# Performance work log

Hardware: AMD Instinct MI355X
Metric: run time of the kernel (lower is better)

## Reference

```python
import jax, jax.numpy as jnp
import numpy as np

B, N, D, H = 4, 1024, 512, 8
DH = D // H  # per-head dim for V and for each of the two Q/K halves
LAM = 0.5


def setup_inputs() -> dict:
    key = jax.random.key(0)
    ks = jax.random.split(key, 7)
    s = 0.02
    return {
        "x": jax.random.normal(ks[0], (B, N, D), dtype=jnp.float32),
        "Wq": jax.random.normal(ks[1], (D, 2 * D), dtype=jnp.float32) * s,
        "bq": jax.random.normal(ks[2], (2 * D,), dtype=jnp.float32) * s,
        "Wk": jax.random.normal(ks[3], (D, 2 * D), dtype=jnp.float32) * s,
        "bk": jax.random.normal(ks[4], (2 * D,), dtype=jnp.float32) * s,
        "Wv": jax.random.normal(ks[5], (D, D), dtype=jnp.float32) * s,
        "bv": jax.random.normal(ks[6], (D,), dtype=jnp.float32) * s,
    }


def reference(x, Wq, bq, Wk, bk, Wv, bv):
    b, n, d = x.shape
    q = (x @ Wq + bq).reshape(b, n, H, 2 * DH).transpose(0, 2, 1, 3)  # [B,H,N,2*DH]
    k = (x @ Wk + bk).reshape(b, n, H, 2 * DH).transpose(0, 2, 1, 3)
    v = (x @ Wv + bv).reshape(b, n, H, DH).transpose(0, 2, 1, 3)      # [B,H,N,DH]
    q1, q2 = q[..., :DH], q[..., DH:]
    k1, k2 = k[..., :DH], k[..., DH:]
    scale = 1.0 / jnp.sqrt(jnp.float32(DH))
    a1 = jax.nn.softmax(jnp.einsum("bhqd,bhkd->bhqk", q1, k1) * scale, axis=-1)
    a2 = jax.nn.softmax(jnp.einsum("bhqd,bhkd->bhqk", q2, k2) * scale, axis=-1)
    attn = a1 - LAM * a2                                              # [B,H,N,N]
    out = jnp.einsum("bhqk,bhkd->bhqd", attn, v)                      # [B,H,N,DH]
    return out.transpose(0, 2, 1, 3).reshape(b, n, d)
```

## Files before the change

kernel.cpp:

```cpp
#include <hip/hip_runtime.h>
#include <hip/hip_bf16.h>

typedef unsigned short u16;
typedef short s16x8 __attribute__((ext_vector_type(8)));
typedef float f32x4 __attribute__((ext_vector_type(4)));

__device__ inline u16 f2bf(float f) {
  union { float f; unsigned int u; } v; v.f = f;
  unsigned int r = v.u + 0x7fffu + ((v.u >> 16) & 1u);
  return (u16)(r >> 16);
}

__device__ __forceinline__ void g2lds16(const u16* g, u16* l) {
  __builtin_amdgcn_global_load_lds((const __attribute__((address_space(1))) void*)g,
                                   (__attribute__((address_space(3))) void*)l, 16, 0, 0);
}

__global__ __launch_bounds__(256) void cast_x_kernel(const float* __restrict__ x,
                                                     u16* __restrict__ xb) {
  int i = (blockIdx.x * 256 + threadIdx.x) * 8;
  float4 a = *(const float4*)(x + i);
  float4 b = *(const float4*)(x + i + 4);
  s16x8 o;
  o[0] = (short)f2bf(a.x); o[1] = (short)f2bf(a.y);
  o[2] = (short)f2bf(a.z); o[3] = (short)f2bf(a.w);
  o[4] = (short)f2bf(b.x); o[5] = (short)f2bf(b.y);
  o[6] = (short)f2bf(b.z); o[7] = (short)f2bf(b.w);
  *(s16x8*)(xb + i) = o;
}

__global__ __launch_bounds__(256) void transpose_cast_w(const float* __restrict__ src, int C,
                                                        int rowoff, u16* __restrict__ wt) {
  __shared__ float tile[64][65];
  int j0 = blockIdx.x * 64, k0 = blockIdx.y * 64;
  int tx = threadIdx.x % 64, ty4 = threadIdx.x / 64;
#pragma unroll
  for (int p = 0; p < 16; ++p) {
    int r = p * 4 + ty4;
    tile[r][tx] = src[(size_t)(k0 + r) * C + j0 + tx];
  }
  __syncthreads();
#pragma unroll
  for (int p = 0; p < 16; ++p) {
    int r = p * 4 + ty4;
    wt[(size_t)(rowoff + j0 + r) * 512 + k0 + tx] = f2bf(tile[tx][r]);
  }
}

__global__ __launch_bounds__(256, 2) void gemm_qkv(const u16* __restrict__ xb, const u16* __restrict__ wt,
                                                   const float* __restrict__ bq, const float* __restrict__ bk,
                                                   const float* __restrict__ bv,
                                                   u16* __restrict__ qa, u16* __restrict__ ka,
                                                   u16* __restrict__ va) {
  __shared__ __align__(16) u16 As[128 * 64];
  __shared__ __align__(16) u16 Bs[128 * 64];
  int m0 = blockIdx.x * 128, j0 = blockIdx.y * 128;
  int tid = threadIdx.x;
  int w = tid >> 6, lane = tid & 63, quad = lane >> 4, l16 = lane & 15;
  int wr = (w >> 1) * 64, wc = (w & 1) * 64;

  int srow[4], scol[4], sbase[4];
#pragma unroll
  for (int it = 0; it < 4; ++it) {
    int s = it * 256 + tid;
    srow[it] = s >> 3;
    scol[it] = (s & 7) ^ ((s >> 3) & 7);
    sbase[it] = (s & ~63) * 8;
  }

  f32x4 acc[4][4];
#pragma unroll
  for (int i = 0; i < 4; ++i)
#pragma unroll
    for (int j = 0; j < 4; ++j)
#pragma unroll
      for (int r = 0; r < 4; ++r) acc[i][j][r] = 0.f;

  for (int kk = 0; kk < 8; ++kk) {
    int k0 = kk * 64;
    __syncthreads();
#pragma unroll
    for (int it = 0; it < 4; ++it) {
      g2lds16(xb + (size_t)(m0 + srow[it]) * 512 + k0 + scol[it] * 8, &As[sbase[it]]);
      g2lds16(wt + (size_t)(j0 + srow[it]) * 512 + k0 + scol[it] * 8, &Bs[sbase[it]]);
    }
    __syncthreads();
#pragma unroll
    for (int kb = 0; kb < 2; ++kb) {
      s16x8 af[4], bfr[4];
#pragma unroll
      for (int rb = 0; rb < 4; ++rb) {
        int row = wr + rb * 16 + l16;
        af[rb] = *(const s16x8*)(&As[row * 64 + (((kb * 4 + quad) ^ (row & 7)) * 8)]);
      }
#pragma unroll
      for (int cb = 0; cb < 4; ++cb) {
        int row = wc + cb * 16 + l16;
        bfr[cb] = *(const s16x8*)(&Bs[row * 64 + (((kb * 4 + quad) ^ (row & 7)) * 8)]);
      }
#pragma unroll
      for (int rb = 0; rb < 4; ++rb)
#pragma unroll
        for (int cb = 0; cb < 4; ++cb)
          acc[rb][cb] = __builtin_amdgcn_mfma_f32_16x16x32_bf16(af[rb], bfr[cb], acc[rb][cb], 0, 0, 0);
    }
  }

#pragma unroll
  for (int cb = 0; cb < 4; ++cb) {
    int j = j0 + wc + cb * 16 + l16;
    float bias = (j < 1024) ? bq[j] : (j < 2048) ? bk[j - 1024] : bv[j - 2048];
#pragma unroll
    for (int rb = 0; rb < 4; ++rb) {
#pragma unroll
      for (int r = 0; r < 4; ++r) {
        int m = m0 + wr + rb * 16 + quad * 4 + r;
        int bidx = m >> 10, n = m & 1023;
        u16 o = f2bf(acc[rb][cb][r] + bias);
        if (j < 1024) {
          int h = j >> 7, r2 = j & 127;
          qa[((size_t)((bidx * 8 + h) * 1024 + n)) * 128 + r2] = o;
        } else if (j < 2048) {
          int jj = j - 1024, h = jj >> 7, r2 = jj & 127;
          ka[((size_t)((bidx * 8 + h) * 1024 + n)) * 128 + r2] = o;
        } else {
          int jj = j - 2048, h = jj >> 6, d = jj & 63;
          va[((size_t)((bidx * 8 + h) * 64 + d)) * 1024 + n] = o;
        }
      }
    }
  }
}

__global__ __launch_bounds__(256, 2) void attn_kernel(const u16* __restrict__ qa, const u16* __restrict__ ka,
                                                      const u16* __restrict__ va, float* __restrict__ out) {
  __shared__ __align__(16) u16 Ks[2][64 * 128];
  __shared__ __align__(16) u16 Vs[2][64 * 64];
  __shared__ __align__(16) u16 Ps[2][64 * 72];
  int bh = blockIdx.x, b = bh >> 3, h = bh & 7;
  int q0 = blockIdx.y * 64;
  int tid = threadIdx.x, w = tid >> 6, lane = tid & 63, quad = lane >> 4, l16 = lane & 15;

  const u16* qrow = qa + (size_t)(bh * 1024 + q0 + w * 16 + l16) * 128;
  s16x8 qf[2][2];
  qf[0][0] = *(const s16x8*)(qrow + quad * 8);
  qf[0][1] = *(const s16x8*)(qrow + 32 + quad * 8);
  qf[1][0] = *(const s16x8*)(qrow + 64 + quad * 8);
  qf[1][1] = *(const s16x8*)(qrow + 96 + quad * 8);

  f32x4 O1[5], O2[5];
#pragma unroll
  for (int i = 0; i < 5; ++i)
#pragma unroll
    for (int r = 0; r < 4; ++r) { O1[i][r] = 0.f; O2[i][r] = 0.f; }

  s16x8 onesf;
#pragma unroll
  for (int i = 0; i < 8; ++i) onesf[i] = (l16 == 0) ? (short)0x3F80 : (short)0;

  int krow[4], kcol[4], kbse[4];
#pragma unroll
  for (int it = 0; it < 4; ++it) {
    int s = it * 256 + tid;
    krow[it] = s >> 4; kcol[it] = (s & 15) ^ ((s >> 4) & 7); kbse[it] = (s & ~63) * 8;
  }
  int vrow[2], vcol[2], vbse[2];
#pragma unroll
  for (int it = 0; it < 2; ++it) {
    int s = it * 256 + tid;
    vrow[it] = s >> 3; vcol[it] = (s & 7) ^ ((s >> 3) & 7); vbse[it] = (s & ~63) * 8;
  }
  const u16* kgbase = ka + (size_t)bh * 1024 * 128;
  const u16* vgbase = va + (size_t)bh * 64 * 1024;

  auto stage = [&](int kt, int bufi) {
    int n0 = kt * 64;
#pragma unroll
    for (int it = 0; it < 4; ++it)
      g2lds16(kgbase + (size_t)(n0 + krow[it]) * 128 + kcol[it] * 8, &Ks[bufi][kbse[it]]);
#pragma unroll
    for (int it = 0; it < 2; ++it)
      g2lds16(vgbase + (size_t)vrow[it] * 1024 + n0 + vcol[it] * 8, &Vs[bufi][vbse[it]]);
  };

  stage(0, 0);
  __syncthreads();

  for (int kt = 0; kt < 16; ++kt) {
    int cur = kt & 1;
    if (kt < 15) stage(kt + 1, cur ^ 1);

    s16x8 vf[4][2];
#pragma unroll
    for (int ct = 0; ct < 4; ++ct)
#pragma unroll
      for (int kb = 0; kb < 2; ++kb) {
        int row = ct * 16 + l16;
        vf[ct][kb] = *(const s16x8*)(&Vs[cur][row * 64 + (((kb * 4 + quad) ^ (row & 7)) * 8)]);
      }

#pragma unroll
    for (int hh = 0; hh < 2; ++hh) {
#pragma unroll
      for (int nt = 0; nt < 4; ++nt) {
        f32x4 sv; sv[0] = sv[1] = sv[2] = sv[3] = 0.f;
#pragma unroll
        for (int kb = 0; kb < 2; ++kb) {
          int row = nt * 16 + l16;
          s16x8 kf = *(const s16x8*)(&Ks[cur][row * 128 + (((hh * 8 + kb * 4 + quad) ^ (row & 7)) * 8)]);
          sv = __builtin_amdgcn_mfma_f32_16x16x32_bf16(qf[hh][kb], kf, sv, 0, 0, 0);
        }
#pragma unroll
        for (int r = 0; r < 4; ++r)
          Ps[hh][(w * 16 + quad * 4 + r) * 72 + nt * 16 + l16] = f2bf(__expf(sv[r] * 0.125f));
      }
    }
    asm volatile("s_waitcnt lgkmcnt(0)" ::: "memory");
    s16x8 pf[2][2];
#pragma unroll
    for (int hh = 0; hh < 2; ++hh) {
      pf[hh][0] = *(const s16x8*)(&Ps[hh][(w * 16 + l16) * 72 + quad * 8]);
      pf[hh][1] = *(const s16x8*)(&Ps[hh][(w * 16 + l16) * 72 + 32 + quad * 8]);
    }
#pragma unroll
    for (int ct = 0; ct < 5; ++ct) {
      s16x8 b0 = (ct < 4) ? vf[ct][0] : onesf;
      s16x8 b1 = (ct < 4) ? vf[ct][1] : onesf;
      O1[ct] = __builtin_amdgcn_mfma_f32_16x16x32_bf16(pf[0][0], b0, O1[ct], 0, 0, 0);
      O1[ct] = __builtin_amdgcn_mfma_f32_16x16x32_bf16(pf[0][1], b1, O1[ct], 0, 0, 0);
      O2[ct] = __builtin_amdgcn_mfma_f32_16x16x32_bf16(pf[1][0], b0, O2[ct], 0, 0, 0);
      O2[ct] = __builtin_amdgcn_mfma_f32_16x16x32_bf16(pf[1][1], b1, O2[ct], 0, 0, 0);
    }
    __syncthreads();
  }

  float inv1[4], inv2[4];
#pragma unroll
  for (int r = 0; r < 4; ++r) {
    float l1 = __shfl(O1[4][r], lane & 48, 64);
    float l2 = __shfl(O2[4][r], lane & 48, 64);
    inv1[r] = 1.0f / l1;
    inv2[r] = 1.0f / l2;
  }
  int nb = q0 + w * 16 + quad * 4;
#pragma unroll
  for (int ct = 0; ct < 4; ++ct)
#pragma unroll
    for (int r = 0; r < 4; ++r) {
      float val = O1[ct][r] * inv1[r] - 0.5f * O2[ct][r] * inv2[r];
      out[(size_t)(b * 1024 + nb + r) * 512 + h * 64 + ct * 16 + l16] = val;
    }
}

extern "C" void kernel_launch(void* const* d_in, const int* in_sizes, int n_in,
                              void* d_out, int out_size, void* d_ws, size_t ws_size,
                              hipStream_t stream) {
  (void)in_sizes; (void)n_in; (void)out_size; (void)ws_size;
  const float* x  = (const float*)d_in[0];
  const float* Wq = (const float*)d_in[1];
  const float* bq = (const float*)d_in[2];
  const float* Wk = (const float*)d_in[3];
  const float* bk = (const float*)d_in[4];
  const float* Wv = (const float*)d_in[5];
  const float* bv = (const float*)d_in[6];
  float* out = (float*)d_out;

  char* ws = (char*)d_ws;
  u16* xb = (u16*)(ws);
  u16* wt = (u16*)(ws + 4194304);
  u16* qa = (u16*)(ws + 6815744);
  u16* ka = (u16*)(ws + 15204352);
  u16* va = (u16*)(ws + 23592960);

  cast_x_kernel<<<1024, 256, 0, stream>>>(x, xb);
  transpose_cast_w<<<dim3(16, 8), 256, 0, stream>>>(Wq, 1024, 0, wt);
  transpose_cast_w<<<dim3(16, 8), 256, 0, stream>>>(Wk, 1024, 1024, wt);
  transpose_cast_w<<<dim3(8, 8), 256, 0, stream>>>(Wv, 512, 2048, wt);
  gemm_qkv<<<dim3(32, 20), 256, 0, stream>>>(xb, wt, bq, bk, bv, qa, ka, va);
  attn_kernel<<<dim3(32, 16), 256, 0, stream>>>(qa, ka, va, out);
}
```

Measured before the change: 139.2 us.

## Split attention KV across warps, double-buffer GEMM, merge weight transposes

The attention kernel now processes 32 query rows per block, with the two warp pairs each covering half of every 64-key tile. It stages K/V through registers into a single LDS buffer and reduces the two partial accumulators through shared memory at the end. The launch grid doubles and launch bounds allow 3 blocks per CU, aiming to raise occupancy. The QKV GEMM gains double-buffered LDS so the next K-slab loads during MFMA work, and the three weight transpose launches are merged into one 3D-grid launch. The trade-offs are more LDS reduction and sync work, a larger LDS footprint in the GEMM, and half the per-warp MFMA work on each K tile.

```diff
diff --git a/kernel.cpp b/kernel.cpp
--- a/kernel.cpp
+++ b/kernel.cpp
@@ -29,8 +29,15 @@
   *(s16x8*)(xb + i) = o;
 }
 
-__global__ __launch_bounds__(256) void transpose_cast_w(const float* __restrict__ src, int C,
-                                                        int rowoff, u16* __restrict__ wt) {
+__global__ __launch_bounds__(256) void transpose_cast_w3(const float* __restrict__ Wq,
+                                                         const float* __restrict__ Wk,
+                                                         const float* __restrict__ Wv,
+                                                         u16* __restrict__ wt) {
+  int z = blockIdx.z;
+  if (z == 2 && blockIdx.x >= 8) return;
+  const float* src = (z == 0) ? Wq : (z == 1) ? Wk : Wv;
+  int C = (z == 2) ? 512 : 1024;
+  int rowoff = z * 1024;
   __shared__ float tile[64][65];
   int j0 = blockIdx.x * 64, k0 = blockIdx.y * 64;
   int tx = threadIdx.x % 64, ty4 = threadIdx.x / 64;
@@ -52,8 +59,8 @@
                                                    const float* __restrict__ bv,
                                                    u16* __restrict__ qa, u16* __restrict__ ka,
                                                    u16* __restrict__ va) {
-  __shared__ __align__(16) u16 As[128 * 64];
-  __shared__ __align__(16) u16 Bs[128 * 64];
+  __shared__ __align__(16) u16 As[2][128 * 64];
+  __shared__ __align__(16) u16 Bs[2][128 * 64];
   int m0 = blockIdx.x * 128, j0 = blockIdx.y * 128;
   int tid = threadIdx.x;
   int w = tid >> 6, lane = tid & 63, quad = lane >> 4, l16 = lane & 15;
@@ -76,27 +83,32 @@
 #pragma unroll
       for (int r = 0; r < 4; ++r) acc[i][j][r] = 0.f;
 
+  auto stage = [&](int kk, int bi) {
+    int k0 = kk * 64;
+#pragma unroll
+    for (int it = 0; it < 4; ++it) {
+      g2lds16(xb + (size_t)(m0 + srow[it]) * 512 + k0 + scol[it] * 8, &As[bi][sbase[it]]);
+      g2lds16(wt + (size_t)(j0 + srow[it]) * 512 + k0 + scol[it] * 8, &Bs[bi][sbase[it]]);
+    }
+  };
+
+  stage(0, 0);
   for (int kk = 0; kk < 8; ++kk) {
-    int k0 = kk * 64;
     __syncthreads();
-#pragma unroll
-    for (int it = 0; it < 4; ++it) {
-      g2lds16(xb + (size_t)(m0 + srow[it]) * 512 + k0 + scol[it] * 8, &As[sbase[it]]);
-      g2lds16(wt + (size_t)(j0 + srow[it]) * 512 + k0 + scol[it] * 8, &Bs[sbase[it]]);
-    }
-    __syncthreads();
+    if (kk < 7) stage(kk + 1, (kk + 1) & 1);
+    int bi = kk & 1;
 #pragma unroll
     for (int kb = 0; kb < 2; ++kb) {
       s16x8 af[4], bfr[4];
 #pragma unroll
       for (int rb = 0; rb < 4; ++rb) {
         int row = wr + rb * 16 + l16;
-        af[rb] = *(const s16x8*)(&As[row * 64 + (((kb * 4 + quad) ^ (row & 7)) * 8)]);
+        af[rb] = *(const s16x8*)(&As[bi][row * 64 + (((kb * 4 + quad) ^ (row & 7)) * 8)]);
       }
 #pragma unroll
       for (int cb = 0; cb < 4; ++cb) {
         int row = wc + cb * 16 + l16;
-        bfr[cb] = *(const s16x8*)(&Bs[row * 64 + (((kb * 4 + quad) ^ (row & 7)) * 8)]);
+        bfr[cb] = *(const s16x8*)(&Bs[bi][row * 64 + (((kb * 4 + quad) ^ (row & 7)) * 8)]);
       }
 #pragma unroll
       for (int rb = 0; rb < 4; ++rb)
@@ -132,16 +144,24 @@
   }
 }
 
-__global__ __launch_bounds__(256, 2) void attn_kernel(const u16* __restrict__ qa, const u16* __restrict__ ka,
+__global__ __launch_bounds__(256, 3) void attn_kernel(const u16* __restrict__ qa, const u16* __restrict__ ka,
                                                       const u16* __restrict__ va, float* __restrict__ out) {
-  __shared__ __align__(16) u16 Ks[2][64 * 128];
-  __shared__ __align__(16) u16 Vs[2][64 * 64];
-  __shared__ __align__(16) u16 Ps[2][64 * 72];
+  __shared__ __align__(16) u16 smem[17408];
+  u16* Ks = smem;
+  u16* Vs = smem + 8192;
+  u16* Ps = smem + 12288;
+  float* Ex = (float*)smem;
+
   int bh = blockIdx.x, b = bh >> 3, h = bh & 7;
-  int q0 = blockIdx.y * 64;
+  int q0 = blockIdx.y * 32;
   int tid = threadIdx.x, w = tid >> 6, lane = tid & 63, quad = lane >> 4, l16 = lane & 15;
-
-  const u16* qrow = qa + (size_t)(bh * 1024 + q0 + w * 16 + l16) * 128;
+  int kh = w >> 1;
+  int qr = q0 + (w & 1) * 16;
+
+  const u16* kgbase = ka + (size_t)bh * 1024 * 128;
+  const u16* vgbase = va + (size_t)bh * 64 * 1024;
+
+  const u16* qrow = qa + (size_t)(bh * 1024 + qr + l16) * 128;
   s16x8 qf[2][2];
   qf[0][0] = *(const s16x8*)(qrow + quad * 8);
   qf[0][1] = *(const s16x8*)(qrow + 32 + quad * 8);
@@ -158,98 +178,128 @@
 #pragma unroll
   for (int i = 0; i < 8; ++i) onesf[i] = (l16 == 0) ? (short)0x3F80 : (short)0;
 
-  int krow[4], kcol[4], kbse[4];
-#pragma unroll
-  for (int it = 0; it < 4; ++it) {
-    int s = it * 256 + tid;
-    krow[it] = s >> 4; kcol[it] = (s & 15) ^ ((s >> 4) & 7); kbse[it] = (s & ~63) * 8;
-  }
-  int vrow[2], vcol[2], vbse[2];
-#pragma unroll
-  for (int it = 0; it < 2; ++it) {
-    int s = it * 256 + tid;
-    vrow[it] = s >> 3; vcol[it] = (s & 7) ^ ((s >> 3) & 7); vbse[it] = (s & ~63) * 8;
-  }
-  const u16* kgbase = ka + (size_t)bh * 1024 * 128;
-  const u16* vgbase = va + (size_t)bh * 64 * 1024;
-
-  auto stage = [&](int kt, int bufi) {
-    int n0 = kt * 64;
-#pragma unroll
-    for (int it = 0; it < 4; ++it)
-      g2lds16(kgbase + (size_t)(n0 + krow[it]) * 128 + kcol[it] * 8, &Ks[bufi][kbse[it]]);
-#pragma unroll
-    for (int it = 0; it < 2; ++it)
-      g2lds16(vgbase + (size_t)vrow[it] * 1024 + n0 + vcol[it] * 8, &Vs[bufi][vbse[it]]);
-  };
-
-  stage(0, 0);
-  __syncthreads();
+  int kго_dummy = 0; (void)kго_dummy;
+  int kldso[4]; size_t kgo[4];
+#pragma unroll
+  for (int i = 0; i < 4; ++i) {
+    int s = i * 256 + tid;
+    int skh = s >> 9, r = s & 511, row = r >> 4, c = r & 15;
+    kldso[i] = skh * 4096 + row * 128 + ((c ^ (row & 7)) * 8);
+    kgo[i] = (size_t)(skh * 512 + row) * 128 + c * 8;
+  }
+  int vldso[2]; size_t vgo[2];
+#pragma unroll
+  for (int i = 0; i < 2; ++i) {
+    int s = i * 256 + tid;
+    int skh = s >> 8, r = s & 255, row = r >> 2, c = r & 3;
+    vldso[i] = skh * 2048 + row * 32 + ((c ^ (row & 3)) * 8);
+    vgo[i] = (size_t)row * 1024 + skh * 512 + c * 8;
+  }
+
+  int4 kreg[4], vreg[2];
+#pragma unroll
+  for (int i = 0; i < 4; ++i) kreg[i] = *(const int4*)(kgbase + kgo[i]);
+#pragma unroll
+  for (int i = 0; i < 2; ++i) vreg[i] = *(const int4*)(vgbase + vgo[i]);
 
   for (int kt = 0; kt < 16; ++kt) {
-    int cur = kt & 1;
-    if (kt < 15) stage(kt + 1, cur ^ 1);
-
-    s16x8 vf[4][2];
-#pragma unroll
-    for (int ct = 0; ct < 4; ++ct)
-#pragma unroll
-      for (int kb = 0; kb < 2; ++kb) {
-        int row = ct * 16 + l16;
-        vf[ct][kb] = *(const s16x8*)(&Vs[cur][row * 64 + (((kb * 4 + quad) ^ (row & 7)) * 8)]);
-      }
+#pragma unroll
+    for (int i = 0; i < 4; ++i) *(int4*)(&Ks[kldso[i]]) = kreg[i];
+#pragma unroll
+    for (int i = 0; i < 2; ++i) *(int4*)(&Vs[vldso[i]]) = vreg[i];
+    __syncthreads();
+    int ktn = (kt < 15) ? kt + 1 : 15;
+#pragma unroll
+    for (int i = 0; i < 4; ++i) kreg[i] = *(const int4*)(kgbase + kgo[i] + (size_t)ktn * 4096);
+#pragma unroll
+    for (int i = 0; i < 2; ++i) vreg[i] = *(const int4*)(vgbase + vgo[i] + (size_t)ktn * 32);
+
+    s16x8 vf[4];
+#pragma unroll
+    for (int ct = 0; ct < 4; ++ct) {
+      int row = ct * 16 + l16;
+      vf[ct] = *(const s16x8*)(&Vs[kh * 2048 + row * 32 + ((quad ^ (row & 3)) * 8)]);
+    }
 
 #pragma unroll
     for (int hh = 0; hh < 2; ++hh) {
 #pragma unroll
-      for (int nt = 0; nt < 4; ++nt) {
+      for (int nt = 0; nt < 2; ++nt) {
         f32x4 sv; sv[0] = sv[1] = sv[2] = sv[3] = 0.f;
 #pragma unroll
         for (int kb = 0; kb < 2; ++kb) {
           int row = nt * 16 + l16;
-          s16x8 kf = *(const s16x8*)(&Ks[cur][row * 128 + (((hh * 8 + kb * 4 + quad) ^ (row & 7)) * 8)]);
+          s16x8 kf = *(const s16x8*)(&Ks[kh * 4096 + row * 128 +
+                                         (((hh * 8 + kb * 4 + quad) ^ (row & 7)) * 8)]);
           sv = __builtin_amdgcn_mfma_f32_16x16x32_bf16(qf[hh][kb], kf, sv, 0, 0, 0);
         }
 #pragma unroll
         for (int r = 0; r < 4; ++r)
-          Ps[hh][(w * 16 + quad * 4 + r) * 72 + nt * 16 + l16] = f2bf(__expf(sv[r] * 0.125f));
+          Ps[((w * 2 + hh) * 16 + quad * 4 + r) * 40 + nt * 16 + l16] = f2bf(__expf(sv[r] * 0.125f));
       }
     }
     asm volatile("s_waitcnt lgkmcnt(0)" ::: "memory");
-    s16x8 pf[2][2];
-#pragma unroll
-    for (int hh = 0; hh < 2; ++hh) {
-      pf[hh][0] = *(const s16x8*)(&Ps[hh][(w * 16 + l16) * 72 + quad * 8]);
-      pf[hh][1] = *(const s16x8*)(&Ps[hh][(w * 16 + l16) * 72 + 32 + quad * 8]);
-    }
+    s16x8 pf0 = *(const s16x8*)(&Ps[((w * 2 + 0) * 16 + l16) * 40 + quad * 8]);
+    s16x8 pf1 = *(const s16x8*)(&Ps[((w * 2 + 1) * 16 + l16) * 40 + quad * 8]);
 #pragma unroll
     for (int ct = 0; ct < 5; ++ct) {
-      s16x8 b0 = (ct < 4) ? vf[ct][0] : onesf;
-      s16x8 b1 = (ct < 4) ? vf[ct][1] : onesf;
-      O1[ct] = __builtin_amdgcn_mfma_f32_16x16x32_bf16(pf[0][0], b0, O1[ct], 0, 0, 0);
-      O1[ct] = __builtin_amdgcn_mfma_f32_16x16x32_bf16(pf[0][1], b1, O1[ct], 0, 0, 0);
-      O2[ct] = __builtin_amdgcn_mfma_f32_16x16x32_bf16(pf[1][0], b0, O2[ct], 0, 0, 0);
-      O2[ct] = __builtin_amdgcn_mfma_f32_16x16x32_bf16(pf[1][1], b1, O2[ct], 0, 0, 0);
+      s16x8 bfr = (ct < 4) ? vf[ct] : onesf;
+      O1[ct] = __builtin_amdgcn_mfma_f32_16x16x32_bf16(pf0, bfr, O1[ct], 0, 0, 0);
+      O2[ct] = __builtin_amdgcn_mfma_f32_16x16x32_bf16(pf1, bfr, O2[ct], 0, 0, 0);
     }
     __syncthreads();
   }
 
-  float inv1[4], inv2[4];
-#pragma unroll
-  for (int r = 0; r < 4; ++r) {
-    float l1 = __shfl(O1[4][r], lane & 48, 64);
-    float l2 = __shfl(O2[4][r], lane & 48, 64);
-    inv1[r] = 1.0f / l1;
-    inv2[r] = 1.0f / l2;
-  }
-  int nb = q0 + w * 16 + quad * 4;
-#pragma unroll
-  for (int ct = 0; ct < 4; ++ct)
+  if (w >= 2) {
+    int wi = w - 2;
+#pragma unroll
+    for (int ct = 0; ct < 4; ++ct)
+#pragma unroll
+      for (int r = 0; r < 4; ++r) {
+        Ex[((wi * 2 + 0) * 16 + quad * 4 + r) * 68 + ct * 16 + l16] = O1[ct][r];
+        Ex[((wi * 2 + 1) * 16 + quad * 4 + r) * 68 + ct * 16 + l16] = O2[ct][r];
+      }
+    if (l16 == 0) {
+#pragma unroll
+      for (int r = 0; r < 4; ++r) {
+        Ex[((wi * 2 + 0) * 16 + quad * 4 + r) * 68 + 64] = O1[4][r];
+        Ex[((wi * 2 + 1) * 16 + quad * 4 + r) * 68 + 64] = O2[4][r];
+      }
+    }
+  }
+  __syncthreads();
+  if (w < 2) {
+#pragma unroll
+    for (int ct = 0; ct < 4; ++ct)
+#pragma unroll
+      for (int r = 0; r < 4; ++r) {
+        O1[ct][r] += Ex[((w * 2 + 0) * 16 + quad * 4 + r) * 68 + ct * 16 + l16];
+        O2[ct][r] += Ex[((w * 2 + 1) * 16 + quad * 4 + r) * 68 + ct * 16 + l16];
+      }
+    if (l16 == 0) {
+#pragma unroll
+      for (int r = 0; r < 4; ++r) {
+        O1[4][r] += Ex[((w * 2 + 0) * 16 + quad * 4 + r) * 68 + 64];
+        O2[4][r] += Ex[((w * 2 + 1) * 16 + quad * 4 + r) * 68 + 64];
+      }
+    }
+    float inv1[4], inv2[4];
 #pragma unroll
     for (int r = 0; r < 4; ++r) {
-      float val = O1[ct][r] * inv1[r] - 0.5f * O2[ct][r] * inv2[r];
-      out[(size_t)(b * 1024 + nb + r) * 512 + h * 64 + ct * 16 + l16] = val;
-    }
+      float l1 = __shfl(O1[4][r], lane & 48, 64);
+      float l2 = __shfl(O2[4][r], lane & 48, 64);
+      inv1[r] = 1.0f / l1;
+      inv2[r] = 1.0f / l2;
+    }
+    int nb = qr + quad * 4;
+#pragma unroll
+    for (int ct = 0; ct < 4; ++ct)
+#pragma unroll
+      for (int r = 0; r < 4; ++r) {
+        float val = O1[ct][r] * inv1[r] - 0.5f * O2[ct][r] * inv2[r];
+        out[(size_t)(b * 1024 + nb + r) * 512 + h * 64 + ct * 16 + l16] = val;
+      }
+  }
 }
 
 extern "C" void kernel_launch(void* const* d_in, const int* in_sizes, int n_in,
@@ -273,9 +323,7 @@
   u16* va = (u16*)(ws + 23592960);
 
   cast_x_kernel<<<1024, 256, 0, stream>>>(x, xb);
-  transpose_cast_w<<<dim3(16, 8), 256, 0, stream>>>(Wq, 1024, 0, wt);
-  transpose_cast_w<<<dim3(16, 8), 256, 0, stream>>>(Wk, 1024, 1024, wt);
-  transpose_cast_w<<<dim3(8, 8), 256, 0, stream>>>(Wv, 512, 2048, wt);
+  transpose_cast_w3<<<dim3(16, 8, 3), 256, 0, stream>>>(Wq, Wk, Wv, wt);
   gemm_qkv<<<dim3(32, 20), 256, 0, stream>>>(xb, wt, bq, bk, bv, qa, ka, va);
-  attn_kernel<<<dim3(32, 16), 256, 0, stream>>>(qa, ka, va, out);
-}
+  attn_kernel<<<dim3(32, 32), 256, 0, stream>>>(qa, ka, va, out);
+}
```

Result: slower. 221.3 us (+59.0%).
